# Kernel tuning notes

Hardware: AMD Instinct MI355X
Metric: run time of the kernel (lower is better)

The kernel has to match this reference:

```python
import jax, jax.numpy as jnp
import numpy as np
from jax import lax


def setup_inputs() -> dict:
    key = jax.random.key(0)
    ks = jax.random.split(key, 3)
    T, B, IC, HC, L = 512, 64, 1024, 1024, 2
    # xavier_normal-ish scale for square layers
    scale = (2.0 / (IC + HC)) ** 0.5
    x = jax.random.normal(ks[0], (T, B, IC), dtype=jnp.float32)
    Wi = jax.random.normal(ks[1], (L, HC, IC), dtype=jnp.float32) * scale
    Wh = jax.random.normal(ks[2], (L, HC, HC), dtype=jnp.float32) * scale
    bi = jnp.zeros((L, HC), dtype=jnp.float32)
    bh = jnp.zeros((L, HC), dtype=jnp.float32)
    return {"x": x, "Wi": Wi, "bi": bi, "Wh": Wh, "bh": bh}


def _run_rnn(x, Wi, bi, Wh, bh):
    # x: [T, B, ic]; Wi: [L, hc, ic]; Wh: [L, hc, hc]
    L = Wi.shape[0]
    B = x.shape[1]
    HC = Wh.shape[-1]
    seq = x
    finals = []
    for i in range(L):  # small fixed layer count
        # precompute input projection for all timesteps (one big GEMM)
        pre = jnp.einsum('tbi,hi->tbh', seq, Wi[i]) + bi[i]
        Wh_i, bh_i = Wh[i], bh[i]

        def step(h, p):
            h_new = jnp.tanh(p + h @ Wh_i.T + bh_i)
            return h_new, h_new

        h0 = jnp.zeros((B, HC), dtype=x.dtype)  # hiddens=None, learn_init=False
        h_last, seq = lax.scan(step, h0, pre)
        finals.append(h_last)
    hs = jnp.stack(finals, axis=0)  # [L, B, hc]
    return seq, hs


def reference(x, Wi, bi, Wh, bh):
    out, hs = _run_rnn(x, Wi, bi, Wh, bh)
    return out, hs
```

## Files before the change

kernel.cpp:

```cpp
#include <hip/hip_runtime.h>


#define T_STEPS 512
#define HCC     1024
#define BH      65536
#define NWG     192

typedef __attribute__((ext_vector_type(8))) short  bf16x8;
typedef __attribute__((ext_vector_type(4))) float  f32x4;

#define WF_SHORTS   8388608u
#define SLAB_SHORTS 131072u
#define OFF_H1F     WF_SHORTS
#define OFF_H2F     (OFF_H1F + 4u*SLAB_SHORTS)
#define OFF_PRE2_BYTES ((size_t)(OFF_H2F + 4u*SLAB_SHORTS) * 2u)
#define PRE2_FLOATS 65536u
#define FLG_BYTE_OFF (OFF_PRE2_BYTES + 4u*(size_t)PRE2_FLOATS*4u)
#define FLG_UINTS   (3u*64u*4u*4u)

__device__ __forceinline__ unsigned fidx(unsigned g, unsigned i, unsigned wp) {
    return ((g * 64u + i) * 4u + wp) * 4u;
}

__device__ __forceinline__ void gload_b128_cc(bf16x8& d, const unsigned short* p) {
    asm volatile("global_load_dwordx4 %0, %1, off sc0 sc1" : "=v"(d) : "v"(p));
}
__device__ __forceinline__ void gload_f128_cc(f32x4& d, const float* p) {
    asm volatile("global_load_dwordx4 %0, %1, off sc0 sc1" : "=v"(d) : "v"(p));
}
__device__ __forceinline__ void gload_f128_nc(f32x4& d, const float* p) {
    asm volatile("global_load_dwordx4 %0, %1, off" : "=v"(d) : "v"(p));
}
__device__ __forceinline__ void gstore_b128_cc(bf16x8 v, unsigned short* p) {
    asm volatile("global_store_dwordx4 %0, %1, off sc0 sc1" :: "v"(p), "v"(v) : "memory");
}
__device__ __forceinline__ void gstore_f128_cc(f32x4 v, float* p) {
    asm volatile("global_store_dwordx4 %0, %1, off sc0 sc1" :: "v"(p), "v"(v) : "memory");
}
__device__ __forceinline__ void vm_drain()  { asm volatile("s_waitcnt vmcnt(0)"  ::: "memory"); }
__device__ __forceinline__ void vm_wait8()  { asm volatile("s_waitcnt vmcnt(8)"  ::: "memory"); }
#define SBAR() __builtin_amdgcn_sched_barrier(0)

__device__ __forceinline__ unsigned short bf16_rne_bits(float f) {
    unsigned u = __builtin_bit_cast(unsigned, f);
    unsigned r = u + 0x7fffu + ((u >> 16) & 1u);
    return (unsigned short)(r >> 16);
}
__device__ __forceinline__ void split1(float f, unsigned short& hi, unsigned short& lo) {
    unsigned u = __builtin_bit_cast(unsigned, f);
    unsigned r = (u + 0x7fffu + ((u >> 16) & 1u)) & 0xffff0000u;
    hi = (unsigned short)(r >> 16);
    float res = f - __builtin_bit_cast(float, r);
    lo = bf16_rne_bits(res);
}
__device__ __forceinline__ void split8(const float* f, bf16x8& H, bf16x8& L) {
#pragma unroll
    for (int e = 0; e < 8; ++e) {
        unsigned short hi, lo; split1(f[e], hi, lo);
        H[e] = (short)hi; L[e] = (short)lo;
    }
}
__device__ __forceinline__ float tanh_fast(float v) {
    float e = __expf(2.0f * v);
    return 1.0f - 2.0f * __builtin_amdgcn_rcpf(e + 1.0f);
}

__global__ __launch_bounds__(256) void zero_cnt_kernel(unsigned* cnt, unsigned n) {
    unsigned i = blockIdx.x * 256u + threadIdx.x;
    if (i < n) cnt[i] = 0u;
}

__global__ __launch_bounds__(256) void wsplit_kernel(
    const float* __restrict__ Wi, const float* __restrict__ Wh,
    unsigned short* __restrict__ WF)
{
    unsigned id  = blockIdx.x * 256u + threadIdx.x;
    unsigned kc  = id & 127u;
    unsigned row = (id >> 7) & 1023u;
    unsigned m   = id >> 17;

    const float* src = ((m & 1u) ? Wh : Wi) + (size_t)(m >> 1) * HCC * HCC
                     + (size_t)row * HCC + kc * 8u;
    float f[8];
    *(f32x4*)&f[0] = *(const f32x4*)&src[0];
    *(f32x4*)&f[4] = *(const f32x4*)&src[4];
    bf16x8 H, L; split8(f, H, L);

    unsigned c16 = row >> 4, ks = kc >> 2;
    unsigned lane = (row & 15u) + 16u * (kc & 3u);
    size_t bh_ = (((size_t)(m * 2u + 0u) * 64u + c16) * 32u + ks) * 512u + lane * 8u;
    size_t bl_ = (((size_t)(m * 2u + 1u) * 64u + c16) * 32u + ks) * 512u + lane * 8u;
    *(bf16x8*)&WF[bh_] = H;
    *(bf16x8*)&WF[bl_] = L;
}

__global__ __launch_bounds__(256) void pre1_gemm(
    const float* __restrict__ x, const float* __restrict__ bi, const float* __restrict__ bh,
    const unsigned short* __restrict__ WF, float* __restrict__ preO)
{
    __shared__ float xs[64 * 36];
    const unsigned t = blockIdx.x >> 3, cg = blockIdx.x & 7u;
    const unsigned tid = threadIdx.x, w = tid >> 6, lane = tid & 63u;
    const unsigned ct32 = cg * 4u + w;

    float b0 = bi[ct32 * 32u + (lane & 15u)]        + bh[ct32 * 32u + (lane & 15u)];
    float b1 = bi[ct32 * 32u + 16u + (lane & 15u)]  + bh[ct32 * 32u + 16u + (lane & 15u)];
    f32x4 acc[4][2];
#pragma unroll
    for (unsigned rt = 0; rt < 4; ++rt) {
        acc[rt][0] = (f32x4){b0, b0, b0, b0};
        acc[rt][1] = (f32x4){b1, b1, b1, b1};
    }
    const float* xt = x + (size_t)t * BH;

    for (unsigned ks = 0; ks < 32; ++ks) {
        {
            unsigned row = tid >> 2, c8 = (tid & 3u) * 8u;
            const float* sp = xt + (size_t)row * HCC + ks * 32u + c8;
            *(f32x4*)&xs[row * 36u + c8]      = *(const f32x4*)&sp[0];
            *(f32x4*)&xs[row * 36u + c8 + 4u] = *(const f32x4*)&sp[4];
        }
        __syncthreads();
        bf16x8 bhv[2], blv[2];
#pragma unroll
        for (unsigned c16 = 0; c16 < 2; ++c16) {
            size_t base = (((size_t)(0u) * 64u + (ct32 * 2u + c16)) * 32u + ks) * 512u + lane * 8u;
            bhv[c16] = *(const bf16x8*)&WF[base];
            blv[c16] = *(const bf16x8*)&WF[base + (size_t)64u * 32u * 512u];
        }
#pragma unroll
        for (unsigned rt = 0; rt < 4; ++rt) {
            unsigned row = rt * 16u + (lane & 15u);
            unsigned k0 = (lane >> 4) * 8u;
            float f[8];
            *(f32x4*)&f[0] = *(const f32x4*)&xs[row * 36u + k0];
            *(f32x4*)&f[4] = *(const f32x4*)&xs[row * 36u + k0 + 4u];
            bf16x8 ah, al; split8(f, ah, al);
#pragma unroll
            for (unsigned c16 = 0; c16 < 2; ++c16) {
                acc[rt][c16] = __builtin_amdgcn_mfma_f32_16x16x32_bf16(ah, bhv[c16], acc[rt][c16], 0, 0, 0);
                acc[rt][c16] = __builtin_amdgcn_mfma_f32_16x16x32_bf16(al, bhv[c16], acc[rt][c16], 0, 0, 0);
                acc[rt][c16] = __builtin_amdgcn_mfma_f32_16x16x32_bf16(ah, blv[c16], acc[rt][c16], 0, 0, 0);
            }
        }
        __syncthreads();
    }
#pragma unroll
    for (unsigned rt = 0; rt < 4; ++rt)
#pragma unroll
        for (unsigned c16 = 0; c16 < 2; ++c16) {
            unsigned rh = rt >> 1, fi = (rt & 1u) * 2u + c16;
            size_t off = ((((size_t)t * 2u + rh) * 32u + ct32) * 4u + fi) * 256u + lane * 4u;
            *(f32x4*)&preO[off] = acc[rt][c16];
        }
}

__global__ __launch_bounds__(512, 1) void rnn_persist(
    const float* __restrict__ bi, const float* __restrict__ bh,
    const unsigned short* __restrict__ WF,
    unsigned short* __restrict__ h1F, unsigned short* __restrict__ h2F,
    float* __restrict__ pre2F, unsigned* __restrict__ flg,
    float* __restrict__ seqO, float* __restrict__ hsO)
{
    __shared__ short WlS[65536];
    __shared__ float redS[7168];

    const unsigned wg  = blockIdx.x;
    const unsigned grp = wg >> 6;
    const unsigned sub = wg & 63u;
    const unsigned rh  = sub >> 5, ct = sub & 31u;
    const unsigned tid = threadIdx.x;
    const unsigned w   = tid >> 6, lane = tid & 63u;

    const unsigned mat = grp + 1u;
#pragma unroll
    for (unsigned prec = 0; prec < 2; ++prec)
#pragma unroll
        for (unsigned c16l = 0; c16l < 2; ++c16l) {
            const unsigned short* sp = WF + (((size_t)(mat * 2u + prec) * 64u + (ct * 2u + c16l)) * 32u) * 512u;
            short* dp = &WlS[(prec * 2u + c16l) * 16384u];
            for (unsigned o = tid * 8u; o < 16384u; o += 4096u)
                *(bf16x8*)&dp[o] = *(const bf16x8*)&sp[o];
        }
    __syncthreads();

    float bsel = 0.f;
    if (grp == 1u && w < 4u) {
        unsigned c = HCC + ct * 32u + (w & 1u) * 16u + (lane & 15u);
        bsel = bi[c] + bh[c];
    }

    const int s0_ = (grp == 0u) ? 0 : (grp == 1u) ? 1 : 2;
    const int s1_ = s0_ + 511;

#define POLL16(G, TGT) do {                                                           \
        const unsigned* fp_ = flg + fidx((G), rh * 32u + w * 4u + ((lane >> 2) & 3u), \
                                         lane & 3u);                                  \
        while (!__all((int)(__hip_atomic_load(fp_, __ATOMIC_RELAXED,                  \
                                              __HIP_MEMORY_SCOPE_AGENT) >= (unsigned)(TGT)))) \
            __builtin_amdgcn_s_sleep(1);                                              \
    } while (0)
#define POLLW0(G, TGT) do {                                                           \
        const unsigned* fp_ = flg + fidx((G), lane, 0u);                              \
        while (!__all((int)(__hip_atomic_load(fp_, __ATOMIC_RELAXED,                  \
                                              __HIP_MEMORY_SCOPE_AGENT) >= (unsigned)(TGT)))) \
            __builtin_amdgcn_s_sleep(1);                                              \
    } while (0)
#define POLLG1(TGT) do {                                                              \
        const unsigned* fp_ = flg + fidx(1u, sub, lane & 3u);                         \
        while (!__all((int)(__hip_atomic_load(fp_, __ATOMIC_RELAXED,                  \
                                              __HIP_MEMORY_SCOPE_AGENT) >= (unsigned)(TGT)))) \
            __builtin_amdgcn_s_sleep(1);                                              \
    } while (0)

    for (int s = s0_; s <= s1_; ++s) {
        const bool do_h   = (grp == 0u) ? (s > 0) : (grp == 1u) ? true : (s > 2);

        f32x4 ldq = {0, 0, 0, 0};
        if (grp == 0u) {
            if (w < 4u) {
                const float* pp = seqO + (((size_t)s * 2u + rh) * 32u + ct) * 1024u;
                gload_f128_nc(ldq, pp + w * 256u + lane * 4u);
            }
            if (s >= 1) POLL16(0u, s);
        } else if (grp == 1u) {
            POLL16(0u, s);
        } else {
            if (w < 4u) {
                POLLG1(s);
                const float* pp = pre2F + (size_t)((s - 2) & 3) * PRE2_FLOATS
                                + ((size_t)rh * 32u + ct) * 1024u;
                gload_f128_cc(ldq, pp + w * 256u + lane * 4u);
            }
            if (s >= 3) POLL16(2u, s);
        }

        bf16x8 Ah0[4], Ah1[4], Al0[4], Al1[4];
        if (do_h) {
            const unsigned aslot = (grp == 2u) ? ((unsigned)(s - 3) & 3u)
                                               : ((unsigned)(s - 1) & 3u);
            const unsigned short* Aslab = (grp <= 1u ? h1F : h2F)
                                        + (size_t)aslot * SLAB_SHORTS;
            const unsigned b00 = ((rh * 2u + 0u) * 2u + 0u) * 16384u;
            const unsigned b01 = ((rh * 2u + 0u) * 2u + 1u) * 16384u;
            const unsigned b10 = ((rh * 2u + 1u) * 2u + 0u) * 16384u;
            const unsigned b11 = ((rh * 2u + 1u) * 2u + 1u) * 16384u;
#pragma unroll
            for (unsigned i = 0; i < 4; ++i) {
                const unsigned ao = (w * 4u + i) * 512u + lane * 8u;
                gload_b128_cc(Ah0[i], Aslab + b00 + ao);
                gload_b128_cc(Ah1[i], Aslab + b01 + ao);
            }
#pragma unroll
            for (unsigned i = 0; i < 4; ++i) {
                const unsigned ao = (w * 4u + i) * 512u + lane * 8u;
                gload_b128_cc(Al0[i], Aslab + b10 + ao);
                gload_b128_cc(Al1[i], Aslab + b11 + ao);
            }
        }

        f32x4 a00 = {0,0,0,0}, a01 = {0,0,0,0}, a10 = {0,0,0,0}, a11 = {0,0,0,0};
        if (do_h) {
            vm_wait8(); SBAR();
#pragma unroll
            for (unsigned i = 0; i < 4; ++i) {
                const unsigned ao = (w * 4u + i) * 512u + lane * 8u;
                bf16x8 bh0 = *(const bf16x8*)&WlS[ao];
                bf16x8 bh1 = *(const bf16x8*)&WlS[16384u + ao];
                bf16x8 bl0 = *(const bf16x8*)&WlS[32768u + ao];
                bf16x8 bl1 = *(const bf16x8*)&WlS[49152u + ao];
                a00 = __builtin_amdgcn_mfma_f32_16x16x32_bf16(Ah0[i], bh0, a00, 0, 0, 0);
                a01 = __builtin_amdgcn_mfma_f32_16x16x32_bf16(Ah0[i], bh1, a01, 0, 0, 0);
                a10 = __builtin_amdgcn_mfma_f32_16x16x32_bf16(Ah1[i], bh0, a10, 0, 0, 0);
                a11 = __builtin_amdgcn_mfma_f32_16x16x32_bf16(Ah1[i], bh1, a11, 0, 0, 0);
                a00 = __builtin_amdgcn_mfma_f32_16x16x32_bf16(Ah0[i], bl0, a00, 0, 0, 0);
                a01 = __builtin_amdgcn_mfma_f32_16x16x32_bf16(Ah0[i], bl1, a01, 0, 0, 0);
                a10 = __builtin_amdgcn_mfma_f32_16x16x32_bf16(Ah1[i], bl0, a10, 0, 0, 0);
                a11 = __builtin_amdgcn_mfma_f32_16x16x32_bf16(Ah1[i], bl1, a11, 0, 0, 0);
            }
            vm_drain(); SBAR();
#pragma unroll
            for (unsigned i = 0; i < 4; ++i) {
                const unsigned ao = (w * 4u + i) * 512u + lane * 8u;
                bf16x8 bh0 = *(const bf16x8*)&WlS[ao];
                bf16x8 bh1 = *(const bf16x8*)&WlS[16384u + ao];
                a00 = __builtin_amdgcn_mfma_f32_16x16x32_bf16(Al0[i], bh0, a00, 0, 0, 0);
                a01 = __builtin_amdgcn_mfma_f32_16x16x32_bf16(Al0[i], bh1, a01, 0, 0, 0);
                a10 = __builtin_amdgcn_mfma_f32_16x16x32_bf16(Al1[i], bh0, a10, 0, 0, 0);
                a11 = __builtin_amdgcn_mfma_f32_16x16x32_bf16(Al1[i], bh1, a11, 0, 0, 0);
            }
        } else {
            vm_drain(); SBAR();
        }

        if (w == 1u) {
            if (grp == 0u && s >= 4) POLLW0(1u, s - 2);
            if (grp == 1u && s >= 5) POLLW0(2u, s - 2);
        }
        if (w == 2u) {
            if (grp == 0u && s >= 4) POLLW0(0u, s - 2);
            if (grp == 2u && s >= 6) POLLW0(2u, s - 2);
        }

        {
            f32x4 av[4] = {a00, a01, a10, a11};
#pragma unroll
            for (unsigned f = 0; f < 4; ++f) {
                const bool skip = (w < 4u) && (f == w);
                const unsigned wi = w - ((w > f) ? 1u : 0u);
                if (!skip)
                    *(f32x4*)&redS[(f * 7u + wi) * 256u + lane * 4u] = av[f];
            }
        }
        __syncthreads();

        if (w < 4u) {
            f32x4 acc = (w == 0u) ? a00 : (w == 1u) ? a01 : (w == 2u) ? a10 : a11;
#pragma unroll
            for (unsigned b = 0; b < 7; ++b)
                acc += *(const f32x4*)&redS[(w * 7u + b) * 256u + lane * 4u];
            if (grp == 1u) {
                acc += (f32x4){bsel, bsel, bsel, bsel};
                float* pp = pre2F + (size_t)((s - 1) & 3) * PRE2_FLOATS
                          + ((size_t)rh * 32u + ct) * 1024u;
                gstore_f128_cc(acc, pp + w * 256u + lane * 4u);
                vm_drain();
                if (lane == 0u)
                    __hip_atomic_store(flg + fidx(1u, sub, w), (unsigned)s + 1u,
                                       __ATOMIC_RELAXED, __HIP_MEMORY_SCOPE_AGENT);
            } else {
                acc += ldq;
                const unsigned qb = w * 1792u;
                const unsigned rb = (lane >> 4) * 4u;
#pragma unroll
                for (unsigned rr = 0; rr < 4; ++rr)
                    redS[qb + (rb + rr) * 16u + (lane & 15u)] = tanh_fast(acc[rr]);
            }
        }
        if (grp != 1u) {
            __syncthreads();
            if (w < 4u) {
                const unsigned r16l = w >> 1, prec = w & 1u;
                const unsigned c0 = (lane >> 4) * 8u;
                const unsigned q  = r16l * 2u + (c0 >> 4);
                const unsigned qa = q * 1792u + (lane & 15u) * 16u + (c0 & 15u);
                float f[8];
                *(f32x4*)&f[0] = *(const f32x4*)&redS[qa];
                *(f32x4*)&f[4] = *(const f32x4*)&redS[qa + 4u];
                bf16x8 H, L; split8(f, H, L);
                unsigned short* hdst = (grp == 0u ? h1F : h2F)
                    + (size_t)((unsigned)(grp == 0u ? s : s - 2) & 3u) * SLAB_SHORTS;
                gstore_b128_cc(prec ? L : H,
                    hdst + ((rh * 2u + prec) * 2u + r16l) * 16384u + ct * 512u + lane * 8u);
                vm_drain();
                if (lane == 0u)
                    __hip_atomic_store(flg + fidx(grp, sub, w), (unsigned)s + 1u,
                                       __ATOMIC_RELAXED, __HIP_MEMORY_SCOPE_AGENT);
            }
            if (grp == 2u) {
                const int t2 = s - 2;
#pragma unroll
                for (unsigned pass = 0; pass < 2; ++pass) {
                    const unsigned r = w * 4u + pass * 2u + (lane >> 5);
                    const unsigned c = lane & 31u;
                    const float v = redS[((r >> 4) * 2u + (c >> 4)) * 1792u
                                         + (r & 15u) * 16u + (c & 15u)];
                    seqO[((size_t)t2 * 64u + rh * 32u + r) * 1024u + ct * 32u + c] = v;
                    if (s == 513) hsO[BH + (size_t)(rh * 32u + r) * 1024u + ct * 32u + c] = v;
                }
            }
            if (grp == 0u && s == 511) {
#pragma unroll
                for (unsigned pass = 0; pass < 2; ++pass) {
                    const unsigned r = w * 4u + pass * 2u + (lane >> 5);
                    const unsigned c = lane & 31u;
                    hsO[(size_t)(rh * 32u + r) * 1024u + ct * 32u + c]
                        = redS[((r >> 4) * 2u + (c >> 4)) * 1792u
                               + (r & 15u) * 16u + (c & 15u)];
                }
            }
        }
        __syncthreads();
    }
    vm_drain();
#undef POLL16
#undef POLLW0
#undef POLLG1
}

extern "C" void kernel_launch(void* const* d_in, const int* in_sizes, int n_in,
                              void* d_out, int out_size, void* d_ws, size_t ws_size,
                              hipStream_t stream) {
    const float* x  = (const float*)d_in[0];
    const float* Wi = (const float*)d_in[1];
    const float* bi = (const float*)d_in[2];
    const float* Wh = (const float*)d_in[3];
    const float* bh = (const float*)d_in[4];

    float* seqO = (float*)d_out;
    float* hsO  = seqO + (size_t)T_STEPS * BH;

    unsigned short* wsS = (unsigned short*)d_ws;
    unsigned short* WF  = wsS;
    unsigned short* h1F = wsS + OFF_H1F;
    unsigned short* h2F = wsS + OFF_H2F;
    float* pre2F = (float*)((char*)d_ws + OFF_PRE2_BYTES);
    unsigned* flg = (unsigned*)((char*)d_ws + FLG_BYTE_OFF);

    zero_cnt_kernel<<<(FLG_UINTS + 255u) / 256u, 256, 0, stream>>>(flg, FLG_UINTS);
    wsplit_kernel<<<2048, 256, 0, stream>>>(Wi, Wh, WF);
    pre1_gemm<<<4096, 256, 0, stream>>>(x, bi, bh, WF, seqO);
    rnn_persist<<<NWG, 512, 0, stream>>>(bi, bh, WF, h1F, h2F, pre2F, flg, seqO, hsO);
}
```

Measured before the change: 2.510 ms.

## Fuse layer-1 input projection into persistent RNN kernel as a fourth producer group

The separate pre1_gemm launch is removed. A fourth group of 64 workgroups is added to the persistent kernel; it computes the layer-1 input projection for each timestep with MFMA against Wi held in LDS. It writes the result to seqO and signals per-step flags, which the layer-0 recurrence group polls before loading. The aim is to overlap the input GEMM with the recurrent chain instead of running it up front, at the cost of more resident workgroups, extra flag polling, and a projection that may not keep pace with the recurrence.

New measurement: 3.012 ms. 1.2x slower.

```diff
diff --git a/kernel.cpp b/kernel.cpp
--- a/kernel.cpp
+++ b/kernel.cpp
@@ -4,7 +4,7 @@
 #define T_STEPS 512
 #define HCC     1024
 #define BH      65536
-#define NWG     192
+#define NWG     256
 
 typedef __attribute__((ext_vector_type(8))) short  bf16x8;
 typedef __attribute__((ext_vector_type(4))) float  f32x4;
@@ -16,7 +16,7 @@
 #define OFF_PRE2_BYTES ((size_t)(OFF_H2F + 4u*SLAB_SHORTS) * 2u)
 #define PRE2_FLOATS 65536u
 #define FLG_BYTE_OFF (OFF_PRE2_BYTES + 4u*(size_t)PRE2_FLOATS*4u)
-#define FLG_UINTS   (3u*64u*4u*4u)
+#define FLG_UINTS   (4u*64u*4u*4u)
 
 __device__ __forceinline__ unsigned fidx(unsigned g, unsigned i, unsigned wp) {
     return ((g * 64u + i) * 4u + wp) * 4u;
@@ -94,68 +94,8 @@
     *(bf16x8*)&WF[bl_] = L;
 }
 
-__global__ __launch_bounds__(256) void pre1_gemm(
-    const float* __restrict__ x, const float* __restrict__ bi, const float* __restrict__ bh,
-    const unsigned short* __restrict__ WF, float* __restrict__ preO)
-{
-    __shared__ float xs[64 * 36];
-    const unsigned t = blockIdx.x >> 3, cg = blockIdx.x & 7u;
-    const unsigned tid = threadIdx.x, w = tid >> 6, lane = tid & 63u;
-    const unsigned ct32 = cg * 4u + w;
-
-    float b0 = bi[ct32 * 32u + (lane & 15u)]        + bh[ct32 * 32u + (lane & 15u)];
-    float b1 = bi[ct32 * 32u + 16u + (lane & 15u)]  + bh[ct32 * 32u + 16u + (lane & 15u)];
-    f32x4 acc[4][2];
-#pragma unroll
-    for (unsigned rt = 0; rt < 4; ++rt) {
-        acc[rt][0] = (f32x4){b0, b0, b0, b0};
-        acc[rt][1] = (f32x4){b1, b1, b1, b1};
-    }
-    const float* xt = x + (size_t)t * BH;
-
-    for (unsigned ks = 0; ks < 32; ++ks) {
-        {
-            unsigned row = tid >> 2, c8 = (tid & 3u) * 8u;
-            const float* sp = xt + (size_t)row * HCC + ks * 32u + c8;
-            *(f32x4*)&xs[row * 36u + c8]      = *(const f32x4*)&sp[0];
-            *(f32x4*)&xs[row * 36u + c8 + 4u] = *(const f32x4*)&sp[4];
-        }
-        __syncthreads();
-        bf16x8 bhv[2], blv[2];
-#pragma unroll
-        for (unsigned c16 = 0; c16 < 2; ++c16) {
-            size_t base = (((size_t)(0u) * 64u + (ct32 * 2u + c16)) * 32u + ks) * 512u + lane * 8u;
-            bhv[c16] = *(const bf16x8*)&WF[base];
-            blv[c16] = *(const bf16x8*)&WF[base + (size_t)64u * 32u * 512u];
-        }
-#pragma unroll
-        for (unsigned rt = 0; rt < 4; ++rt) {
-            unsigned row = rt * 16u + (lane & 15u);
-            unsigned k0 = (lane >> 4) * 8u;
-            float f[8];
-            *(f32x4*)&f[0] = *(const f32x4*)&xs[row * 36u + k0];
-            *(f32x4*)&f[4] = *(const f32x4*)&xs[row * 36u + k0 + 4u];
-            bf16x8 ah, al; split8(f, ah, al);
-#pragma unroll
-            for (unsigned c16 = 0; c16 < 2; ++c16) {
-                acc[rt][c16] = __builtin_amdgcn_mfma_f32_16x16x32_bf16(ah, bhv[c16], acc[rt][c16], 0, 0, 0);
-                acc[rt][c16] = __builtin_amdgcn_mfma_f32_16x16x32_bf16(al, bhv[c16], acc[rt][c16], 0, 0, 0);
-                acc[rt][c16] = __builtin_amdgcn_mfma_f32_16x16x32_bf16(ah, blv[c16], acc[rt][c16], 0, 0, 0);
-            }
-        }
-        __syncthreads();
-    }
-#pragma unroll
-    for (unsigned rt = 0; rt < 4; ++rt)
-#pragma unroll
-        for (unsigned c16 = 0; c16 < 2; ++c16) {
-            unsigned rh = rt >> 1, fi = (rt & 1u) * 2u + c16;
-            size_t off = ((((size_t)t * 2u + rh) * 32u + ct32) * 4u + fi) * 256u + lane * 4u;
-            *(f32x4*)&preO[off] = acc[rt][c16];
-        }
-}
-
 __global__ __launch_bounds__(512, 1) void rnn_persist(
+    const float* __restrict__ xin,
     const float* __restrict__ bi, const float* __restrict__ bh,
     const unsigned short* __restrict__ WF,
     unsigned short* __restrict__ h1F, unsigned short* __restrict__ h2F,
@@ -172,7 +112,7 @@
     const unsigned tid = threadIdx.x;
     const unsigned w   = tid >> 6, lane = tid & 63u;
 
-    const unsigned mat = grp + 1u;
+    const unsigned mat = (grp == 3u) ? 0u : (grp + 1u);
 #pragma unroll
     for (unsigned prec = 0; prec < 2; ++prec)
 #pragma unroll
@@ -185,12 +125,12 @@
     __syncthreads();
 
     float bsel = 0.f;
-    if (grp == 1u && w < 4u) {
-        unsigned c = HCC + ct * 32u + (w & 1u) * 16u + (lane & 15u);
+    if ((grp == 1u || grp == 3u) && w < 4u) {
+        unsigned c = (grp == 1u ? HCC : 0u) + ct * 32u + (w & 1u) * 16u + (lane & 15u);
         bsel = bi[c] + bh[c];
     }
 
-    const int s0_ = (grp == 0u) ? 0 : (grp == 1u) ? 1 : 2;
+    const int s0_ = (grp == 1u) ? 1 : (grp == 2u) ? 2 : 0;
     const int s1_ = s0_ + 511;
 
 #define POLL16(G, TGT) do {                                                           \
@@ -212,20 +152,28 @@
                                               __HIP_MEMORY_SCOPE_AGENT) >= (unsigned)(TGT)))) \
             __builtin_amdgcn_s_sleep(1);                                              \
     } while (0)
+#define POLLP(G, IDX, WP, TGT) do {                                                   \
+        const unsigned* fp_ = flg + fidx((G), (IDX), (WP));                           \
+        while (__hip_atomic_load(fp_, __ATOMIC_RELAXED,                               \
+                                 __HIP_MEMORY_SCOPE_AGENT) < (unsigned)(TGT))         \
+            __builtin_amdgcn_s_sleep(1);                                              \
+    } while (0)
 
     for (int s = s0_; s <= s1_; ++s) {
-        const bool do_h   = (grp == 0u) ? (s > 0) : (grp == 1u) ? true : (s > 2);
+        const bool do_h = (grp == 0u) ? (s > 0) : (grp == 1u) ? true
+                        : (grp == 2u) ? (s > 2) : false;
 
         f32x4 ldq = {0, 0, 0, 0};
         if (grp == 0u) {
             if (w < 4u) {
+                POLLP(3u, sub, w, (unsigned)s + 1u);
                 const float* pp = seqO + (((size_t)s * 2u + rh) * 32u + ct) * 1024u;
-                gload_f128_nc(ldq, pp + w * 256u + lane * 4u);
+                gload_f128_cc(ldq, pp + w * 256u + lane * 4u);
             }
             if (s >= 1) POLL16(0u, s);
         } else if (grp == 1u) {
             POLL16(0u, s);
-        } else {
+        } else if (grp == 2u) {
             if (w < 4u) {
                 POLLG1(s);
                 const float* pp = pre2F + (size_t)((s - 2) & 3) * PRE2_FLOATS
@@ -235,6 +183,7 @@
             if (s >= 3) POLL16(2u, s);
         }
 
+        bool do_mm = do_h;
         bf16x8 Ah0[4], Ah1[4], Al0[4], Al1[4];
         if (do_h) {
             const unsigned aslot = (grp == 2u) ? ((unsigned)(s - 3) & 3u)
@@ -257,11 +206,35 @@
                 gload_b128_cc(Al0[i], Aslab + b10 + ao);
                 gload_b128_cc(Al1[i], Aslab + b11 + ao);
             }
+        } else if (grp == 3u) {
+            const float* xt = xin + (size_t)s * BH;
+#pragma unroll
+            for (unsigned r16 = 0; r16 < 2; ++r16) {
+                f32x4 xv[8];
+#pragma unroll
+                for (unsigned i = 0; i < 4; ++i) {
+                    const unsigned row = rh * 32u + r16 * 16u + (lane & 15u);
+                    const unsigned k0  = (w * 4u + i) * 32u + (lane >> 4) * 8u;
+                    gload_f128_nc(xv[i * 2u],      xt + (size_t)row * 1024u + k0);
+                    gload_f128_nc(xv[i * 2u + 1u], xt + (size_t)row * 1024u + k0 + 4u);
+                }
+                vm_drain(); SBAR();
+#pragma unroll
+                for (unsigned i = 0; i < 4; ++i) {
+                    float fb[8];
+                    *(f32x4*)&fb[0] = xv[i * 2u];
+                    *(f32x4*)&fb[4] = xv[i * 2u + 1u];
+                    if (r16 == 0u) split8(fb, Ah0[i], Al0[i]);
+                    else           split8(fb, Ah1[i], Al1[i]);
+                }
+            }
+            do_mm = true;
         }
 
         f32x4 a00 = {0,0,0,0}, a01 = {0,0,0,0}, a10 = {0,0,0,0}, a11 = {0,0,0,0};
-        if (do_h) {
-            vm_wait8(); SBAR();
+        if (do_mm) {
+            if (do_h) vm_wait8();
+            SBAR();
 #pragma unroll
             for (unsigned i = 0; i < 4; ++i) {
                 const unsigned ao = (w * 4u + i) * 512u + lane * 8u;
@@ -278,7 +251,8 @@
                 a10 = __builtin_amdgcn_mfma_f32_16x16x32_bf16(Ah1[i], bl0, a10, 0, 0, 0);
                 a11 = __builtin_amdgcn_mfma_f32_16x16x32_bf16(Ah1[i], bl1, a11, 0, 0, 0);
             }
-            vm_drain(); SBAR();
+            if (do_h) vm_drain();
+            SBAR();
 #pragma unroll
             for (unsigned i = 0; i < 4; ++i) {
                 const unsigned ao = (w * 4u + i) * 512u + lane * 8u;
@@ -328,6 +302,14 @@
                 if (lane == 0u)
                     __hip_atomic_store(flg + fidx(1u, sub, w), (unsigned)s + 1u,
                                        __ATOMIC_RELAXED, __HIP_MEMORY_SCOPE_AGENT);
+            } else if (grp == 3u) {
+                acc += (f32x4){bsel, bsel, bsel, bsel};
+                float* pp = seqO + (((size_t)s * 2u + rh) * 32u + ct) * 1024u;
+                gstore_f128_cc(acc, pp + w * 256u + lane * 4u);
+                vm_drain();
+                if (lane == 0u)
+                    __hip_atomic_store(flg + fidx(3u, sub, w), (unsigned)s + 1u,
+                                       __ATOMIC_RELAXED, __HIP_MEMORY_SCOPE_AGENT);
             } else {
                 acc += ldq;
                 const unsigned qb = w * 1792u;
@@ -337,7 +319,7 @@
                     redS[qb + (rb + rr) * 16u + (lane & 15u)] = tanh_fast(acc[rr]);
             }
         }
-        if (grp != 1u) {
+        if (grp == 0u || grp == 2u) {
             __syncthreads();
             if (w < 4u) {
                 const unsigned r16l = w >> 1, prec = w & 1u;
@@ -386,6 +368,7 @@
 #undef POLL16
 #undef POLLW0
 #undef POLLG1
+#undef POLLP
 }
 
 extern "C" void kernel_launch(void* const* d_in, const int* in_sizes, int n_in,
@@ -409,6 +392,5 @@
 
     zero_cnt_kernel<<<(FLG_UINTS + 255u) / 256u, 256, 0, stream>>>(flg, FLG_UINTS);
     wsplit_kernel<<<2048, 256, 0, stream>>>(Wi, Wh, WF);
-    pre1_gemm<<<4096, 256, 0, stream>>>(x, bi, bh, WF, seqO);
-    rnn_persist<<<NWG, 512, 0, stream>>>(bi, bh, WF, h1F, h2F, pre2F, flg, seqO, hsO);
-}
+    rnn_persist<<<NWG, 512, 0, stream>>>(x, bi, bh, WF, h1F, h2F, pre2F, flg, seqO, hsO);
+}
```
